# Optimization experiments

Measured on AMD Instinct MI355X. Metric: run time of the kernel, lower is better.

Reference implementation:

```python
import jax, jax.numpy as jnp
import numpy as np

D_MODEL = 256
N_LAYERS = 6
N_HEADS = 8
D_FF = 1024
HEAD_DIM = D_MODEL // N_HEADS
EPS = 1e-5


def layer_norm(x, scale, bias):
    mu = jnp.mean(x, axis=-1, keepdims=True)
    var = jnp.var(x, axis=-1, keepdims=True)
    return (x - mu) * jax.lax.rsqrt(var + EPS) * scale + bias


def setup_inputs() -> dict:
    key = jax.random.key(0)
    ks = jax.random.split(key, 12)
    B, T = 4, 2048
    x = jax.random.normal(ks[0], (B, T, D_MODEL), dtype=jnp.float32)
    L = N_LAYERS
    s = 0.02
    inp = {
        "x": x,
        "ln1_s": jnp.ones((L, D_MODEL), jnp.float32),
        "ln1_b": jnp.zeros((L, D_MODEL), jnp.float32),
        "wq": jax.random.normal(ks[1], (L, D_MODEL, D_MODEL), jnp.float32) * s,
        "bq": jnp.zeros((L, D_MODEL), jnp.float32),
        "wk": jax.random.normal(ks[2], (L, D_MODEL, D_MODEL), jnp.float32) * s,
        "bk": jnp.zeros((L, D_MODEL), jnp.float32),
        "wv": jax.random.normal(ks[3], (L, D_MODEL, D_MODEL), jnp.float32) * s,
        "bv": jnp.zeros((L, D_MODEL), jnp.float32),
        "wo": jax.random.normal(ks[4], (L, D_MODEL, D_MODEL), jnp.float32) * s,
        "bo": jnp.zeros((L, D_MODEL), jnp.float32),
        "ln2_s": jnp.ones((L, D_MODEL), jnp.float32),
        "ln2_b": jnp.zeros((L, D_MODEL), jnp.float32),
        "w1": jax.random.normal(ks[5], (L, D_MODEL, D_FF), jnp.float32) * s,
        "b1": jnp.zeros((L, D_FF), jnp.float32),
        "w2": jax.random.normal(ks[6], (L, D_FF, D_MODEL), jnp.float32) * s,
        "b2": jnp.zeros((L, D_MODEL), jnp.float32),
    }
    return inp


def reference(x, ln1_s, ln1_b, wq, bq, wk, bk, wv, bv, wo, bo, ln2_s, ln2_b, w1, b1, w2, b2):
    B, T, D = x.shape
    scale = 1.0 / jnp.sqrt(jnp.float32(HEAD_DIM))
    for l in range(N_LAYERS):
        normed = layer_norm(x, ln1_s[l], ln1_b[l])
        q = (normed @ wq[l] + bq[l]).reshape(B, T, N_HEADS, HEAD_DIM)
        k = (normed @ wk[l] + bk[l]).reshape(B, T, N_HEADS, HEAD_DIM)
        v = (normed @ wv[l] + bv[l]).reshape(B, T, N_HEADS, HEAD_DIM)
        scores = jnp.einsum('bqhd,bkhd->bhqk', q, k) * scale  # [B,H,T,T]
        attn = jax.nn.softmax(scores, axis=-1)
        attn_out = jnp.einsum('bhqk,bkhd->bqhd', attn, v).reshape(B, T, D)
        x = x + attn_out @ wo[l] + bo[l]
        h = layer_norm(x, ln2_s[l], ln2_b[l])
        h = jax.nn.gelu(h @ w1[l] + b1[l], approximate=False)
        x = x + h @ w2[l] + b2[l]
    return x
```

## Files before the change

kernel.cpp:

```cpp
#include <hip/hip_runtime.h>
#include <math.h>

#define D_MODELC 256
#define N_LAYERSC 6
#define N_HEADSC 8
#define D_FFC 1024
#define HEAD_DIMC 32
#define B_SZ 4
#define T_SEQ 2048
#define M_ROWS 8192
#define QKV_N 768
#define KSPLIT 4

typedef short bf16x8 __attribute__((ext_vector_type(8)));
typedef short bf16x4 __attribute__((ext_vector_type(4)));
typedef float f32x4  __attribute__((ext_vector_type(4)));
typedef unsigned u32x4 __attribute__((ext_vector_type(4)));
typedef unsigned short u16;

#define QSCALE 0.25503488f

#define SWZ(b) ((b) ^ (((b) >> 3) & 0x70))

__device__ __forceinline__ void gload16(const void* g, void* l) {
    __builtin_amdgcn_global_load_lds(
        (const __attribute__((address_space(1))) void*)g,
        (__attribute__((address_space(3))) void*)l, 16, 0, 0);
}

__device__ __forceinline__ u16 f2bf(float x) {
    unsigned u = __builtin_bit_cast(unsigned, x);
    u += 0x7FFF + ((u >> 16) & 1);
    return (u16)(u >> 16);
}

__device__ __forceinline__ float bf2f(short x) {
    return __builtin_bit_cast(float, (unsigned)((u16)x) << 16);
}

__device__ __forceinline__ unsigned pack2bf(float a, float b) {
    return __builtin_amdgcn_perm(__builtin_bit_cast(unsigned, b),
                                 __builtin_bit_cast(unsigned, a), 0x07060302u);
}

__device__ __forceinline__ float fast_gelu(float x) {
    float y  = x * 0.70710678118654752f;
    float ay = __builtin_fabsf(y);
    float t  = __builtin_amdgcn_rcpf(1.0f + 0.3275911f * ay);
    float p  = t * (0.254829592f + t * (-0.284496736f + t * (1.421413741f
               + t * (-1.453152027f + t * 1.061405429f))));
    float e  = __builtin_amdgcn_exp2f(-ay * ay * 1.4426950408889634f);
    float er = 1.0f - p * e;
    er = y < 0.0f ? -er : er;
    return 0.5f * x * (1.0f + er);
}

__device__ __forceinline__ void transpose_tile(
    const float* __restrict__ src, u16* __restrict__ dst,
    int K, int N, int k0, int n0, float scale, float (*ts)[33])
{
    const int r = threadIdx.x >> 3, c4 = (threadIdx.x & 7) * 4;
    const float4 v = *(const float4*)(src + (size_t)(k0 + r) * N + n0 + c4);
    ts[r][c4 + 0] = v.x; ts[r][c4 + 1] = v.y;
    ts[r][c4 + 2] = v.z; ts[r][c4 + 3] = v.w;
    __syncthreads();
    bf16x4 o;
#pragma unroll
    for (int i = 0; i < 4; i++) o[i] = (short)f2bf(ts[c4 + i][r] * scale);
    *(bf16x4*)(dst + (size_t)(n0 + r) * K + k0 + c4) = o;
}

__global__ __launch_bounds__(256) void prep_all(
    const float* __restrict__ wq, const float* __restrict__ wk,
    const float* __restrict__ wv, const float* __restrict__ wo,
    const float* __restrict__ w1, const float* __restrict__ w2,
    const float* __restrict__ bq, const float* __restrict__ bk,
    const float* __restrict__ bv,
    u16* __restrict__ wqkv_t, u16* __restrict__ wo_t,
    u16* __restrict__ w1_t, u16* __restrict__ w2_t,
    float* __restrict__ qkvb,
    const float* __restrict__ x, const float* __restrict__ gamma,
    const float* __restrict__ beta, float* __restrict__ X,
    u16* __restrict__ Y)
{
    __shared__ float ts[32][33];
    const int bid = blockIdx.x;
    if (bid < 1152) {
        const int sec = bid / 384, t = bid % 384;
        const int z = t >> 6, rem = t & 63, ty = rem >> 3, tx = rem & 7;
        const float* src = sec == 0 ? wq : (sec == 1 ? wk : wv);
        transpose_tile(src + (size_t)z * 65536,
                       wqkv_t + (size_t)z * QKV_N * 256 + sec * 256 * 256,
                       256, 256, ty * 32, tx * 32,
                       sec == 0 ? QSCALE : 1.0f, ts);
    } else if (bid < 1536) {
        const int t = bid - 1152;
        const int z = t >> 6, rem = t & 63, ty = rem >> 3, tx = rem & 7;
        transpose_tile(wo + (size_t)z * 65536, wo_t + (size_t)z * 65536,
                       256, 256, ty * 32, tx * 32, 1.0f, ts);
    } else if (bid < 3072) {
        const int t = bid - 1536;
        const int z = t >> 8, rem = t & 255, ty = rem >> 5, tx = rem & 31;
        transpose_tile(w1 + (size_t)z * 262144, w1_t + (size_t)z * 262144,
                       256, D_FFC, ty * 32, tx * 32, 1.0f, ts);
    } else if (bid < 4608) {
        const int t = bid - 3072;
        const int z = t >> 8, rem = t & 255, ty = rem >> 3, tx = rem & 7;
        transpose_tile(w2 + (size_t)z * 262144, w2_t + (size_t)z * 262144,
                       D_FFC, 256, ty * 32, tx * 32, 1.0f, ts);
    } else if (bid < 4626) {
        const int i = (bid - 4608) * 256 + threadIdx.x;
        const int l = i / QKV_N, j = i % QKV_N;
        float v;
        if (j < 256)      v = bq[l * 256 + j] * QSCALE;
        else if (j < 512) v = bk[l * 256 + j - 256];
        else              v = bv[l * 256 + j - 512];
        qkvb[i] = v;
    } else {
        const int w = threadIdx.x >> 6, lane = threadIdx.x & 63;
        const int row = (bid - 4626) * 4 + w;
        const float4 v = *(const float4*)(x + (size_t)row * 256 + lane * 4);
        *(float4*)(X + (size_t)row * 256 + lane * 4) = v;
        float sum = v.x + v.y + v.z + v.w;
        float sq  = v.x * v.x + v.y * v.y + v.z * v.z + v.w * v.w;
#pragma unroll
        for (int off = 32; off > 0; off >>= 1) {
            sum += __shfl_xor(sum, off, 64);
            sq  += __shfl_xor(sq,  off, 64);
        }
        float mu  = sum * (1.0f / 256.0f);
        float var = sq * (1.0f / 256.0f) - mu * mu;
        float rr  = rsqrtf(var + 1e-5f);
        const float4 g  = *(const float4*)(gamma + lane * 4);
        const float4 bb = *(const float4*)(beta + lane * 4);
        bf16x4 o;
        o[0] = (short)f2bf((v.x - mu) * rr * g.x + bb.x);
        o[1] = (short)f2bf((v.y - mu) * rr * g.y + bb.y);
        o[2] = (short)f2bf((v.z - mu) * rr * g.z + bb.z);
        o[3] = (short)f2bf((v.w - mu) * rr * g.w + bb.w);
        *(bf16x4*)(Y + (size_t)row * 256 + lane * 4) = o;
    }
}

template <int EPI>
__global__ __launch_bounds__(256) void mfma_gemm(
    const u16* __restrict__ A, const u16* __restrict__ Bt,
    const float* __restrict__ bias, u16* __restrict__ Vout,
    void* __restrict__ Cout, int N, int K)
{
    __shared__ u16 As[128 * 64];
    __shared__ u16 Bs[128 * 64];
    const int tid = threadIdx.x, w = tid >> 6, lane = tid & 63;
    const int c = lane & 15, quad = lane >> 4;
    const int row0 = blockIdx.y * 128, col0 = blockIdx.x * 128;
    const int wr = w >> 1, wc = w & 1;
    const int cswz = (c & 7) << 4;

    int flv[4], rA[4], colA[4];
#pragma unroll
    for (int ci = 0; ci < 4; ci++) {
        flv[ci]  = (w * 4 + ci) * 1024 + lane * 16;
        const int fsw = SWZ(flv[ci]);
        rA[ci]   = fsw >> 7;
        colA[ci] = (fsw & 127) >> 1;
    }

    f32x4 acc[4][4] = {};

    for (int k0 = 0; k0 < K; k0 += 64) {
        __syncthreads();
#pragma unroll
        for (int ci = 0; ci < 4; ci++) {
            gload16(A  + (size_t)(row0 + rA[ci]) * K + k0 + colA[ci],
                    (char*)As + flv[ci]);
            gload16(Bt + (size_t)(col0 + rA[ci]) * K + k0 + colA[ci],
                    (char*)Bs + flv[ci]);
        }
        __syncthreads();
#pragma unroll
        for (int kk = 0; kk < 2; kk++) {
            bf16x8 af[4], bfv[4];
#pragma unroll
            for (int i = 0; i < 4; i++)
                af[i] = *(const bf16x8*)((const char*)As +
                    ((((wr * 64 + i * 16 + c) * 64 + kk * 32 + quad * 8) * 2) ^ cswz));
#pragma unroll
            for (int j = 0; j < 4; j++)
                bfv[j] = *(const bf16x8*)((const char*)Bs +
                    ((((wc * 64 + j * 16 + c) * 64 + kk * 32 + quad * 8) * 2) ^ cswz));
#pragma unroll
            for (int i = 0; i < 4; i++)
#pragma unroll
                for (int j = 0; j < 4; j++)
                    acc[i][j] = __builtin_amdgcn_mfma_f32_16x16x32_bf16(
                        af[i], bfv[j], acc[i][j], 0, 0, 0);
        }
    }

    float bj[4];
#pragma unroll
    for (int j = 0; j < 4; j++) bj[j] = bias[col0 + wc * 64 + j * 16 + c];

    if (EPI == 3 && col0 >= 512) {
#pragma unroll
        for (int i = 0; i < 4; i++) {
            const int tok = row0 + wr * 64 + i * 16 + quad * 4;
#pragma unroll
            for (int j = 0; j < 4; j++) {
                const int dim = col0 - 512 + wc * 64 + j * 16 + c;
                bf16x4 o;
#pragma unroll
                for (int r = 0; r < 4; r++) o[r] = (short)f2bf(acc[i][j][r] + bj[j]);
                *(bf16x4*)&Vout[(size_t)dim * M_ROWS + tok] = o;
            }
        }
        return;
    }

#pragma unroll
    for (int i = 0; i < 4; i++) {
#pragma unroll
        for (int r = 0; r < 4; r++) {
            const int gr = row0 + wr * 64 + i * 16 + quad * 4 + r;
#pragma unroll
            for (int j = 0; j < 4; j++) {
                const int gc = col0 + wc * 64 + j * 16 + c;
                float v = acc[i][j][r] + bj[j];
                if (EPI == 2) v = fast_gelu(v);
                ((u16*)Cout)[(size_t)gr * N + gc] = f2bf(v);
            }
        }
    }
}

template <int DOLN, int MERGE>
__global__ __launch_bounds__(256) void gemm_ln(
    const u16* __restrict__ A, const float* __restrict__ Lmrg,
    const u16* __restrict__ Bt, const float* __restrict__ bias,
    const float* __restrict__ resid, float* __restrict__ Xout,
    const float* __restrict__ gamma, const float* __restrict__ beta,
    u16* __restrict__ Nout, int K)
{
    __shared__ u16 As[32 * 64];
    __shared__ u16 Bs[256 * 64];
    __shared__ float2 red[4][32];
    const int tid = threadIdx.x, w = tid >> 6, lane = tid & 63;
    const int c = lane & 15, quad = lane >> 4;
    const int row0 = blockIdx.x * 32;
    const int cswz = (c & 7) << 4;

    const int flA  = w * 1024 + lane * 16;
    const int fsA  = SWZ(flA);
    const int rA_m = flA >> 7, colA_m = (flA & 127) >> 1;
    const int rA_g = fsA >> 7, colA_g = (fsA & 127) >> 1;

    int flB[8], rB[8], colB[8];
#pragma unroll
    for (int ci = 0; ci < 8; ci++) {
        flB[ci]  = (w * 8 + ci) * 1024 + lane * 16;
        const int fsB = SWZ(flB[ci]);
        rB[ci]   = fsB >> 7;
        colB[ci] = (fsB & 127) >> 1;
    }

    f32x4 acc[2][4] = {};

    auto loadA = [&](int gc) -> bf16x8 {
        const int row = row0 + rA_m;
        const int head = gc >> 5;
        float ls = 0.f;
#pragma unroll
        for (int p = 0; p < KSPLIT; p++)
            ls += Lmrg[(size_t)p * M_ROWS * 8 + (size_t)row * 8 + head];
        const float inv = __builtin_amdgcn_rcpf(ls);
        float s[8] = {0.f, 0.f, 0.f, 0.f, 0.f, 0.f, 0.f, 0.f};
#pragma unroll
        for (int p = 0; p < KSPLIT; p++) {
            bf16x8 a = *(const bf16x8*)(A + (size_t)p * M_ROWS * 256
                                          + (size_t)row * 256 + gc);
#pragma unroll
            for (int j = 0; j < 8; j++) s[j] += bf2f(a[j]);
        }
        bf16x8 o;
#pragma unroll
        for (int j = 0; j < 8; j++) o[j] = (short)f2bf(s[j] * inv);
        return o;
    };

    bf16x8 pA;
    if (MERGE) pA = loadA(colA_m);

    for (int k0 = 0; k0 < K; k0 += 64) {
        __syncthreads();
#pragma unroll
        for (int ci = 0; ci < 8; ci++)
            gload16(Bt + (size_t)rB[ci] * K + k0 + colB[ci], (char*)Bs + flB[ci]);
        if (MERGE) {
            *(bf16x8*)((char*)As + fsA) = pA;
        } else {
            gload16(A + (size_t)(row0 + rA_g) * K + k0 + colA_g, (char*)As + flA);
        }
        __syncthreads();
        if (MERGE && k0 + 64 < K)
            pA = loadA(k0 + 64 + colA_m);
#pragma unroll
        for (int kk = 0; kk < 2; kk++) {
            bf16x8 af[2], bfv[4];
#pragma unroll
            for (int i = 0; i < 2; i++)
                af[i] = *(const bf16x8*)((const char*)As +
                    ((((i * 16 + c) * 64 + kk * 32 + quad * 8) * 2) ^ cswz));
#pragma unroll
            for (int j = 0; j < 4; j++)
                bfv[j] = *(const bf16x8*)((const char*)Bs +
                    ((((w * 64 + j * 16 + c) * 64 + kk * 32 + quad * 8) * 2) ^ cswz));
#pragma unroll
            for (int i = 0; i < 2; i++)
#pragma unroll
                for (int j = 0; j < 4; j++)
                    acc[i][j] = __builtin_amdgcn_mfma_f32_16x16x32_bf16(
                        af[i], bfv[j], acc[i][j], 0, 0, 0);
        }
    }

    float bj[4];
#pragma unroll
    for (int j = 0; j < 4; j++) bj[j] = bias[w * 64 + j * 16 + c];
    float xv[2][4][4];
#pragma unroll
    for (int i = 0; i < 2; i++)
#pragma unroll
        for (int r = 0; r < 4; r++) {
            const int gr = row0 + i * 16 + quad * 4 + r;
#pragma unroll
            for (int j = 0; j < 4; j++) {
                const int gc = w * 64 + j * 16 + c;
                xv[i][j][r] = acc[i][j][r] + bj[j] + resid[(size_t)gr * 256 + gc];
            }
        }

    if (DOLN) {
        float sm[2][4], sp[2][4];
#pragma unroll
        for (int i = 0; i < 2; i++)
#pragma unroll
            for (int r = 0; r < 4; r++) {
                float s = 0.f, q = 0.f;
#pragma unroll
                for (int j = 0; j < 4; j++) { s += xv[i][j][r]; q += xv[i][j][r] * xv[i][j][r]; }
                sm[i][r] = s; sp[i][r] = q;
            }
#pragma unroll
        for (int off = 1; off < 16; off <<= 1)
#pragma unroll
            for (int i = 0; i < 2; i++)
#pragma unroll
                for (int r = 0; r < 4; r++) {
                    sm[i][r] += __shfl_xor(sm[i][r], off, 64);
                    sp[i][r] += __shfl_xor(sp[i][r], off, 64);
                }
        __syncthreads();
        if (c == 0) {
#pragma unroll
            for (int i = 0; i < 2; i++)
#pragma unroll
                for (int r = 0; r < 4; r++)
                    red[w][i * 16 + quad * 4 + r] = make_float2(sm[i][r], sp[i][r]);
        }
        __syncthreads();
#pragma unroll
        for (int i = 0; i < 2; i++)
#pragma unroll
            for (int r = 0; r < 4; r++) {
                const int row = i * 16 + quad * 4 + r;
                float2 t0 = red[0][row], t1 = red[1][row];
                float2 t2 = red[2][row], t3 = red[3][row];
                float S = (t0.x + t1.x) + (t2.x + t3.x);
                float Q = (t0.y + t1.y) + (t2.y + t3.y);
                float mu = S * (1.0f / 256.0f);
                float var = Q * (1.0f / 256.0f) - mu * mu;
                float rr = rsqrtf(var + 1e-5f);
                const int gr = row0 + row;
#pragma unroll
                for (int j = 0; j < 4; j++) {
                    const int gc = w * 64 + j * 16 + c;
                    float x = xv[i][j][r];
                    Xout[(size_t)gr * 256 + gc] = x;
                    Nout[(size_t)gr * 256 + gc] =
                        f2bf((x - mu) * rr * gamma[gc] + beta[gc]);
                }
            }
    } else {
#pragma unroll
        for (int i = 0; i < 2; i++)
#pragma unroll
            for (int r = 0; r < 4; r++) {
                const int gr = row0 + i * 16 + quad * 4 + r;
#pragma unroll
                for (int j = 0; j < 4; j++)
                    Xout[(size_t)gr * 256 + w * 64 + j * 16 + c] = xv[i][j][r];
            }
    }
}

__global__ __launch_bounds__(256) void attn_kernel(
    const u16* __restrict__ QKV, const u16* __restrict__ VT,
    u16* __restrict__ PO, float* __restrict__ Lp)
{
    const int h = blockIdx.y, b = blockIdx.z;
    const int part = blockIdx.x & (KSPLIT - 1);
    const int q0 = (blockIdx.x >> 2) * 128;
    const int tid = threadIdx.x, w = tid >> 6, lane = tid & 63;
    const int c = lane & 15, quad = lane >> 4;

    __shared__ u16 Kf[4096];
    __shared__ u16 Vf[4096];

    const u16* qp = QKV + (size_t)(b * T_SEQ + q0 + w * 32 + c) * QKV_N + h * 32 + quad * 8;
    bf16x8 aQ0 = *(const bf16x8*)qp;
    bf16x8 aQ1 = *(const bf16x8*)(qp + 16 * QKV_N);

    const bf16x8 bOnes = {0x3F80, 0x3F80, 0x3F80, 0x3F80,
                          0x3F80, 0x3F80, 0x3F80, 0x3F80};

    f32x4 O[2][2] = {};
    f32x4 Ol0 = {0.f, 0.f, 0.f, 0.f}, Ol1 = {0.f, 0.f, 0.f, 0.f};

    const u16* kgp = QKV + (size_t)(b * T_SEQ + w * 16 + c) * QKV_N + 256 + h * 32 + quad * 8;
    const u16* vgp = VT + ((size_t)h * 32 + (lane & 31)) * M_ROWS + b * T_SEQ
                     + (w * 2 + (lane >> 5)) * 8;
    u16* kfw = Kf + w * 512 + lane * 8;

    const int vd  = lane & 31, vdh = vd >> 4, vc = vd & 15, vhi = lane >> 5;
    const int vkh = w >> 1, vseg = w & 1;
    const int voff = ((((vkh * 2 + vdh) * 4 + 2 * vhi) * 16 + vc) * 8) + vseg * 4;

    const int kbeg = part * (T_SEQ / KSPLIT);
    const int kend = kbeg + T_SEQ / KSPLIT;

    bf16x8 gK0 = *(const bf16x8*)(kgp + (size_t)kbeg * QKV_N);
    bf16x8 gK1 = *(const bf16x8*)(kgp + (size_t)(kbeg + 64) * QKV_N);
    bf16x8 gV0 = *(const bf16x8*)(vgp + kbeg);
    bf16x8 gV1 = *(const bf16x8*)(vgp + kbeg + 64);

    for (int k0 = kbeg; k0 < kend; k0 += 128) {
        __syncthreads();
        *(bf16x8*)kfw          = gK0;
        *(bf16x8*)(kfw + 2048) = gK1;
        {
            bf16x4 l0v = __builtin_shufflevector(gV0, gV0, 0, 1, 2, 3);
            bf16x4 h0v = __builtin_shufflevector(gV0, gV0, 4, 5, 6, 7);
            bf16x4 l1v = __builtin_shufflevector(gV1, gV1, 0, 1, 2, 3);
            bf16x4 h1v = __builtin_shufflevector(gV1, gV1, 4, 5, 6, 7);
            *(bf16x4*)&Vf[voff]              = l0v;
            *(bf16x4*)&Vf[voff + 128]        = h0v;
            *(bf16x4*)&Vf[2048 + voff]       = l1v;
            *(bf16x4*)&Vf[2048 + voff + 128] = h1v;
        }
        __syncthreads();
        if (k0 + 128 < kend) {
            gK0 = *(const bf16x8*)(kgp + (size_t)(k0 + 128) * QKV_N);
            gK1 = *(const bf16x8*)(kgp + (size_t)(k0 + 192) * QKV_N);
            gV0 = *(const bf16x8*)(vgp + k0 + 128);
            gV1 = *(const bf16x8*)(vgp + k0 + 192);
        }

#pragma unroll
        for (int hf = 0; hf < 2; hf++) {
            const u16* Kb = Kf + hf * 2048;
            const u16* Vb = Vf + hf * 2048;

            unsigned pk0[4][2], pk1[4][2];
#pragma unroll
            for (int g = 0; g < 4; g++) {
                bf16x8 aK = *(const bf16x8*)&Kb[g * 512 + lane * 8];
                f32x4 S0 = __builtin_amdgcn_mfma_f32_16x16x32_bf16(
                    aK, aQ0, (f32x4){0.f, 0.f, 0.f, 0.f}, 0, 0, 0);
                f32x4 S1 = __builtin_amdgcn_mfma_f32_16x16x32_bf16(
                    aK, aQ1, (f32x4){0.f, 0.f, 0.f, 0.f}, 0, 0, 0);
                pk0[g][0] = pack2bf(__builtin_amdgcn_exp2f(S0[0]),
                                    __builtin_amdgcn_exp2f(S0[1]));
                pk0[g][1] = pack2bf(__builtin_amdgcn_exp2f(S0[2]),
                                    __builtin_amdgcn_exp2f(S0[3]));
                pk1[g][0] = pack2bf(__builtin_amdgcn_exp2f(S1[0]),
                                    __builtin_amdgcn_exp2f(S1[1]));
                pk1[g][1] = pack2bf(__builtin_amdgcn_exp2f(S1[2]),
                                    __builtin_amdgcn_exp2f(S1[3]));
            }

            __builtin_amdgcn_s_setprio(1);
#pragma unroll
            for (int kh = 0; kh < 2; kh++) {
                bf16x8 aP0 = __builtin_bit_cast(bf16x8,
                    (u32x4){pk0[2 * kh][0], pk0[2 * kh][1],
                            pk0[2 * kh + 1][0], pk0[2 * kh + 1][1]});
                bf16x8 aP1 = __builtin_bit_cast(bf16x8,
                    (u32x4){pk1[2 * kh][0], pk1[2 * kh][1],
                            pk1[2 * kh + 1][0], pk1[2 * kh + 1][1]});
                Ol0 = __builtin_amdgcn_mfma_f32_16x16x32_bf16(aP0, bOnes, Ol0, 0, 0, 0);
                Ol1 = __builtin_amdgcn_mfma_f32_16x16x32_bf16(aP1, bOnes, Ol1, 0, 0, 0);
#pragma unroll
                for (int dh = 0; dh < 2; dh++) {
                    bf16x8 bV = *(const bf16x8*)&Vb[((kh * 2 + dh) * 64 + lane) * 8];
                    O[0][dh] = __builtin_amdgcn_mfma_f32_16x16x32_bf16(aP0, bV, O[0][dh], 0, 0, 0);
                    O[1][dh] = __builtin_amdgcn_mfma_f32_16x16x32_bf16(aP1, bV, O[1][dh], 0, 0, 0);
                }
            }
            __builtin_amdgcn_s_setprio(0);
        }
    }

    u16* pb = PO + (size_t)part * M_ROWS * 256
              + (size_t)(b * T_SEQ + q0 + w * 32) * 256 + h * 32;
    if (c == 0) {
        float* lb = Lp + (size_t)part * M_ROWS * 8
                    + (size_t)(b * T_SEQ + q0 + w * 32) * 8 + h;
#pragma unroll
        for (int r = 0; r < 4; r++) {
            lb[(size_t)(quad * 4 + r) * 8]      = Ol0[r];
            lb[(size_t)(16 + quad * 4 + r) * 8] = Ol1[r];
        }
    }
#pragma unroll
    for (int r = 0; r < 4; r++) {
        int src = quad * 4 + r;
        pb[(size_t)src * 256 + c]             = f2bf(O[0][0][r]);
        pb[(size_t)src * 256 + 16 + c]        = f2bf(O[0][1][r]);
        pb[(size_t)(16 + src) * 256 + c]      = f2bf(O[1][0][r]);
        pb[(size_t)(16 + src) * 256 + 16 + c] = f2bf(O[1][1][r]);
    }
}

extern "C" void kernel_launch(void* const* d_in, const int* in_sizes, int n_in,
                              void* d_out, int out_size, void* d_ws, size_t ws_size,
                              hipStream_t stream)
{
    const float* x     = (const float*)d_in[0];
    const float* ln1_s = (const float*)d_in[1];
    const float* ln1_b = (const float*)d_in[2];
    const float* wq    = (const float*)d_in[3];
    const float* bq    = (const float*)d_in[4];
    const float* wk    = (const float*)d_in[5];
    const float* bk    = (const float*)d_in[6];
    const float* wv    = (const float*)d_in[7];
    const float* bv    = (const float*)d_in[8];
    const float* wo    = (const float*)d_in[9];
    const float* bo    = (const float*)d_in[10];
    const float* ln2_s = (const float*)d_in[11];
    const float* ln2_b = (const float*)d_in[12];
    const float* w1    = (const float*)d_in[13];
    const float* b1    = (const float*)d_in[14];
    const float* w2    = (const float*)d_in[15];
    const float* b2    = (const float*)d_in[16];

    float* X = (float*)d_out;

    u16* normed = (u16*)d_ws;
    u16* qkv    = normed + (size_t)M_ROWS * 256;
    u16* PO4    = qkv + (size_t)M_ROWS * QKV_N;
    u16* h1     = qkv;
    u16* wqkv_t = PO4 + (size_t)KSPLIT * M_ROWS * 256;
    u16* wo_t   = wqkv_t + (size_t)N_LAYERSC * QKV_N * 256;
    u16* w1_t   = wo_t + (size_t)N_LAYERSC * 256 * 256;
    u16* w2_t   = w1_t + (size_t)N_LAYERSC * D_FFC * 256;
    float* qkvb = (float*)(w2_t + (size_t)N_LAYERSC * 256 * D_FFC);
    u16* VTb    = (u16*)(qkvb + N_LAYERSC * QKV_N);
    float* Lp   = (float*)(VTb + (size_t)256 * M_ROWS);

    dim3 blk(256);

    prep_all<<<dim3(4626 + M_ROWS / 4), blk, 0, stream>>>(
        wq, wk, wv, wo, w1, w2, bq, bk, bv,
        wqkv_t, wo_t, w1_t, w2_t, qkvb,
        x, ln1_s, ln1_b, X, normed);

    dim3 g_qkv(QKV_N / 128, M_ROWS / 128);
    dim3 g_ff(D_FFC / 128, M_ROWS / 128);
    dim3 g_ln32(M_ROWS / 32);
    dim3 g_attn(KSPLIT * T_SEQ / 128, N_HEADSC, B_SZ);

    for (int l = 0; l < N_LAYERSC; l++) {
        mfma_gemm<3><<<g_qkv, blk, 0, stream>>>(
            normed, wqkv_t + (size_t)l * QKV_N * 256, qkvb + l * QKV_N,
            VTb, qkv, QKV_N, 256);
        attn_kernel<<<g_attn, blk, 0, stream>>>(qkv, VTb, PO4, Lp);
        gemm_ln<1, 1><<<g_ln32, blk, 0, stream>>>(
            PO4, Lp, wo_t + (size_t)l * 256 * 256, bo + l * 256, X,
            X, ln2_s + l * 256, ln2_b + l * 256, VTb, 256);
        mfma_gemm<2><<<g_ff, blk, 0, stream>>>(
            VTb, w1_t + (size_t)l * D_FFC * 256, b1 + l * D_FFC,
            nullptr, h1, D_FFC, 256);
        if (l + 1 < N_LAYERSC) {
            gemm_ln<1, 0><<<g_ln32, blk, 0, stream>>>(
                h1, nullptr, w2_t + (size_t)l * 256 * D_FFC,
                b2 + l * 256, X, X, ln1_s + (l + 1) * 256,
                ln1_b + (l + 1) * 256, normed, D_FFC);
        } else {
            gemm_ln<0, 0><<<g_ln32, blk, 0, stream>>>(
                h1, nullptr, w2_t + (size_t)l * 256 * D_FFC,
                b2 + l * 256, X, X, nullptr, nullptr, nullptr, D_FFC);
        }
    }
}
```

Before: 625.8 us.

## Halve attention KV split and widen gemm_ln blocks to 512 threads

Reduces the attention key split from 4 to 2 partitions, halving the partial-output buffer that the output-projection GEMM must read and merge. Separately, gemm_ln now runs with 8 waves per 32-row block, each wave covering 32 output columns instead of 64. This aims to cut merge traffic and raise latency hiding in the LN-fused GEMMs. The cost is fewer attention blocks, with each doing twice the KV work, and an 8-way LN reduction in shared memory.

```diff
diff --git a/kernel.cpp b/kernel.cpp
--- a/kernel.cpp
+++ b/kernel.cpp
@@ -10,7 +10,7 @@
 #define T_SEQ 2048
 #define M_ROWS 8192
 #define QKV_N 768
-#define KSPLIT 4
+#define KSPLIT 2
 
 typedef short bf16x8 __attribute__((ext_vector_type(8)));
 typedef short bf16x4 __attribute__((ext_vector_type(4)));
@@ -234,7 +234,7 @@
 }
 
 template <int DOLN, int MERGE>
-__global__ __launch_bounds__(256) void gemm_ln(
+__global__ __launch_bounds__(512) void gemm_ln(
     const u16* __restrict__ A, const float* __restrict__ Lmrg,
     const u16* __restrict__ Bt, const float* __restrict__ bias,
     const float* __restrict__ resid, float* __restrict__ Xout,
@@ -243,27 +243,28 @@
 {
     __shared__ u16 As[32 * 64];
     __shared__ u16 Bs[256 * 64];
-    __shared__ float2 red[4][32];
+    __shared__ float2 red[8][32];
     const int tid = threadIdx.x, w = tid >> 6, lane = tid & 63;
     const int c = lane & 15, quad = lane >> 4;
     const int row0 = blockIdx.x * 32;
     const int cswz = (c & 7) << 4;
 
-    const int flA  = w * 1024 + lane * 16;
+    const int flA  = tid * 16;
+    const bool doA = tid < 256;
     const int fsA  = SWZ(flA);
     const int rA_m = flA >> 7, colA_m = (flA & 127) >> 1;
     const int rA_g = fsA >> 7, colA_g = (fsA & 127) >> 1;
 
-    int flB[8], rB[8], colB[8];
-#pragma unroll
-    for (int ci = 0; ci < 8; ci++) {
-        flB[ci]  = (w * 8 + ci) * 1024 + lane * 16;
+    int flB[4], rB[4], colB[4];
+#pragma unroll
+    for (int ci = 0; ci < 4; ci++) {
+        flB[ci]  = (w * 4 + ci) * 1024 + lane * 16;
         const int fsB = SWZ(flB[ci]);
         rB[ci]   = fsB >> 7;
         colB[ci] = (fsB & 127) >> 1;
     }
 
-    f32x4 acc[2][4] = {};
+    f32x4 acc[2][2] = {};
 
     auto loadA = [&](int gc) -> bf16x8 {
         const int row = row0 + rA_m;
@@ -288,53 +289,54 @@
     };
 
     bf16x8 pA;
-    if (MERGE) pA = loadA(colA_m);
+    if (MERGE && doA) pA = loadA(colA_m);
 
     for (int k0 = 0; k0 < K; k0 += 64) {
         __syncthreads();
 #pragma unroll
-        for (int ci = 0; ci < 8; ci++)
+        for (int ci = 0; ci < 4; ci++)
             gload16(Bt + (size_t)rB[ci] * K + k0 + colB[ci], (char*)Bs + flB[ci]);
         if (MERGE) {
-            *(bf16x8*)((char*)As + fsA) = pA;
+            if (doA) *(bf16x8*)((char*)As + fsA) = pA;
         } else {
-            gload16(A + (size_t)(row0 + rA_g) * K + k0 + colA_g, (char*)As + flA);
-        }
-        __syncthreads();
-        if (MERGE && k0 + 64 < K)
+            if (doA) gload16(A + (size_t)(row0 + rA_g) * K + k0 + colA_g,
+                             (char*)As + flA);
+        }
+        __syncthreads();
+        if (MERGE && doA && k0 + 64 < K)
             pA = loadA(k0 + 64 + colA_m);
 #pragma unroll
         for (int kk = 0; kk < 2; kk++) {
-            bf16x8 af[2], bfv[4];
+            bf16x8 af[2], bfv[2];
 #pragma unroll
             for (int i = 0; i < 2; i++)
                 af[i] = *(const bf16x8*)((const char*)As +
                     ((((i * 16 + c) * 64 + kk * 32 + quad * 8) * 2) ^ cswz));
 #pragma unroll
-            for (int j = 0; j < 4; j++)
+            for (int j = 0; j < 2; j++)
                 bfv[j] = *(const bf16x8*)((const char*)Bs +
-                    ((((w * 64 + j * 16 + c) * 64 + kk * 32 + quad * 8) * 2) ^ cswz));
+                    ((((w * 32 + j * 16 + c) * 64 + kk * 32 + quad * 8) * 2) ^ cswz));
 #pragma unroll
             for (int i = 0; i < 2; i++)
 #pragma unroll
-                for (int j = 0; j < 4; j++)
+                for (int j = 0; j < 2; j++)
                     acc[i][j] = __builtin_amdgcn_mfma_f32_16x16x32_bf16(
                         af[i], bfv[j], acc[i][j], 0, 0, 0);
         }
     }
 
-    float bj[4];
-#pragma unroll
-    for (int j = 0; j < 4; j++) bj[j] = bias[w * 64 + j * 16 + c];
-    float xv[2][4][4];
+    float bj[2];
+#pragma unroll
+    for (int j = 0; j < 2; j++) bj[j] = bias[w * 32 + j * 16 + c];
+    float xv[2][2][4];
 #pragma unroll
     for (int i = 0; i < 2; i++)
 #pragma unroll
         for (int r = 0; r < 4; r++) {
             const int gr = row0 + i * 16 + quad * 4 + r;
 #pragma unroll
-            for (int j = 0; j < 4; j++) {
-                const int gc = w * 64 + j * 16 + c;
+            for (int j = 0; j < 2; j++) {
+                const int gc = w * 32 + j * 16 + c;
                 xv[i][j][r] = acc[i][j][r] + bj[j] + resid[(size_t)gr * 256 + gc];
             }
         }
@@ -347,7 +349,7 @@
             for (int r = 0; r < 4; r++) {
                 float s = 0.f, q = 0.f;
 #pragma unroll
-                for (int j = 0; j < 4; j++) { s += xv[i][j][r]; q += xv[i][j][r] * xv[i][j][r]; }
+                for (int j = 0; j < 2; j++) { s += xv[i][j][r]; q += xv[i][j][r] * xv[i][j][r]; }
                 sm[i][r] = s; sp[i][r] = q;
             }
 #pragma unroll
@@ -373,17 +375,19 @@
 #pragma unroll
             for (int r = 0; r < 4; r++) {
                 const int row = i * 16 + quad * 4 + r;
-                float2 t0 = red[0][row], t1 = red[1][row];
-                float2 t2 = red[2][row], t3 = red[3][row];
-                float S = (t0.x + t1.x) + (t2.x + t3.x);
-                float Q = (t0.y + t1.y) + (t2.y + t3.y);
+                float S = 0.f, Q = 0.f;
+#pragma unroll
+                for (int wp = 0; wp < 8; wp++) {
+                    S += red[wp][row].x;
+                    Q += red[wp][row].y;
+                }
                 float mu = S * (1.0f / 256.0f);
                 float var = Q * (1.0f / 256.0f) - mu * mu;
                 float rr = rsqrtf(var + 1e-5f);
                 const int gr = row0 + row;
 #pragma unroll
-                for (int j = 0; j < 4; j++) {
-                    const int gc = w * 64 + j * 16 + c;
+                for (int j = 0; j < 2; j++) {
+                    const int gc = w * 32 + j * 16 + c;
                     float x = xv[i][j][r];
                     Xout[(size_t)gr * 256 + gc] = x;
                     Nout[(size_t)gr * 256 + gc] =
@@ -397,8 +401,8 @@
             for (int r = 0; r < 4; r++) {
                 const int gr = row0 + i * 16 + quad * 4 + r;
 #pragma unroll
-                for (int j = 0; j < 4; j++)
-                    Xout[(size_t)gr * 256 + w * 64 + j * 16 + c] = xv[i][j][r];
+                for (int j = 0; j < 2; j++)
+                    Xout[(size_t)gr * 256 + w * 32 + j * 16 + c] = xv[i][j][r];
             }
     }
 }
@@ -409,7 +413,7 @@
 {
     const int h = blockIdx.y, b = blockIdx.z;
     const int part = blockIdx.x & (KSPLIT - 1);
-    const int q0 = (blockIdx.x >> 2) * 128;
+    const int q0 = (blockIdx.x >> 1) * 128;
     const int tid = threadIdx.x, w = tid >> 6, lane = tid & 63;
     const int c = lane & 15, quad = lane >> 4;
 
@@ -557,9 +561,9 @@
 
     u16* normed = (u16*)d_ws;
     u16* qkv    = normed + (size_t)M_ROWS * 256;
-    u16* PO4    = qkv + (size_t)M_ROWS * QKV_N;
+    u16* PO2    = qkv + (size_t)M_ROWS * QKV_N;
     u16* h1     = qkv;
-    u16* wqkv_t = PO4 + (size_t)KSPLIT * M_ROWS * 256;
+    u16* wqkv_t = PO2 + (size_t)KSPLIT * M_ROWS * 256;
     u16* wo_t   = wqkv_t + (size_t)N_LAYERSC * QKV_N * 256;
     u16* w1_t   = wo_t + (size_t)N_LAYERSC * 256 * 256;
     u16* w2_t   = w1_t + (size_t)N_LAYERSC * D_FFC * 256;
@@ -567,7 +571,7 @@
     u16* VTb    = (u16*)(qkvb + N_LAYERSC * QKV_N);
     float* Lp   = (float*)(VTb + (size_t)256 * M_ROWS);
 
-    dim3 blk(256);
+    dim3 blk(256), blk512(512);
 
     prep_all<<<dim3(4626 + M_ROWS / 4), blk, 0, stream>>>(
         wq, wk, wv, wo, w1, w2, bq, bk, bv,
@@ -583,20 +587,20 @@
         mfma_gemm<3><<<g_qkv, blk, 0, stream>>>(
             normed, wqkv_t + (size_t)l * QKV_N * 256, qkvb + l * QKV_N,
             VTb, qkv, QKV_N, 256);
-        attn_kernel<<<g_attn, blk, 0, stream>>>(qkv, VTb, PO4, Lp);
-        gemm_ln<1, 1><<<g_ln32, blk, 0, stream>>>(
-            PO4, Lp, wo_t + (size_t)l * 256 * 256, bo + l * 256, X,
+        attn_kernel<<<g_attn, blk, 0, stream>>>(qkv, VTb, PO2, Lp);
+        gemm_ln<1, 1><<<g_ln32, blk512, 0, stream>>>(
+            PO2, Lp, wo_t + (size_t)l * 256 * 256, bo + l * 256, X,
             X, ln2_s + l * 256, ln2_b + l * 256, VTb, 256);
         mfma_gemm<2><<<g_ff, blk, 0, stream>>>(
             VTb, w1_t + (size_t)l * D_FFC * 256, b1 + l * D_FFC,
             nullptr, h1, D_FFC, 256);
         if (l + 1 < N_LAYERSC) {
-            gemm_ln<1, 0><<<g_ln32, blk, 0, stream>>>(
+            gemm_ln<1, 0><<<g_ln32, blk512, 0, stream>>>(
                 h1, nullptr, w2_t + (size_t)l * 256 * D_FFC,
                 b2 + l * 256, X, X, ln1_s + (l + 1) * 256,
                 ln1_b + (l + 1) * 256, normed, D_FFC);
         } else {
-            gemm_ln<0, 0><<<g_ln32, blk, 0, stream>>>(
+            gemm_ln<0, 0><<<g_ln32, blk512, 0, stream>>>(
                 h1, nullptr, w2_t + (size_t)l * 256 * D_FFC,
                 b2 + l * 256, X, X, nullptr, nullptr, nullptr, D_FFC);
         }
```

Measured after the change: 614.8 us. Within noise of the previous version (-1.8%).

## Halve attention KV split and shrink gemm_ln row tile to 16

Applied to the files above, without the earlier changes.

Attention now splits the key range in two parts instead of four, which halves the partial output and log-sum buffers that the merged output-projection GEMM has to read and combine. The fused GEMM+LayerNorm kernel now handles 16 rows per block instead of 32, doubling the grid to 512 blocks so more CUs are busy. The cost is that each block reuses the 256-wide weight tile over fewer rows, and only half the threads load A. Attention also exposes less parallelism per head.

```diff
diff --git a/kernel.cpp b/kernel.cpp
--- a/kernel.cpp
+++ b/kernel.cpp
@@ -10,7 +10,7 @@
 #define T_SEQ 2048
 #define M_ROWS 8192
 #define QKV_N 768
-#define KSPLIT 4
+#define KSPLIT 2
 
 typedef short bf16x8 __attribute__((ext_vector_type(8)));
 typedef short bf16x4 __attribute__((ext_vector_type(4)));
@@ -241,15 +241,16 @@
     const float* __restrict__ gamma, const float* __restrict__ beta,
     u16* __restrict__ Nout, int K)
 {
-    __shared__ u16 As[32 * 64];
+    __shared__ u16 As[16 * 64];
     __shared__ u16 Bs[256 * 64];
-    __shared__ float2 red[4][32];
+    __shared__ float2 red[4][16];
     const int tid = threadIdx.x, w = tid >> 6, lane = tid & 63;
     const int c = lane & 15, quad = lane >> 4;
-    const int row0 = blockIdx.x * 32;
+    const int row0 = blockIdx.x * 16;
     const int cswz = (c & 7) << 4;
 
-    const int flA  = w * 1024 + lane * 16;
+    const int flA  = tid * 16;
+    const bool doA = tid < 128;
     const int fsA  = SWZ(flA);
     const int rA_m = flA >> 7, colA_m = (flA & 127) >> 1;
     const int rA_g = fsA >> 7, colA_g = (fsA & 127) >> 1;
@@ -263,7 +264,7 @@
         colB[ci] = (fsB & 127) >> 1;
     }
 
-    f32x4 acc[2][4] = {};
+    f32x4 acc[4] = {};
 
     auto loadA = [&](int gc) -> bf16x8 {
         const int row = row0 + rA_m;
@@ -288,7 +289,7 @@
     };
 
     bf16x8 pA;
-    if (MERGE) pA = loadA(colA_m);
+    if (MERGE && doA) pA = loadA(colA_m);
 
     for (int k0 = 0; k0 < K; k0 += 64) {
         __syncthreads();
@@ -296,110 +297,95 @@
         for (int ci = 0; ci < 8; ci++)
             gload16(Bt + (size_t)rB[ci] * K + k0 + colB[ci], (char*)Bs + flB[ci]);
         if (MERGE) {
-            *(bf16x8*)((char*)As + fsA) = pA;
+            if (doA) *(bf16x8*)((char*)As + fsA) = pA;
         } else {
-            gload16(A + (size_t)(row0 + rA_g) * K + k0 + colA_g, (char*)As + flA);
-        }
-        __syncthreads();
-        if (MERGE && k0 + 64 < K)
+            if (doA) gload16(A + (size_t)(row0 + rA_g) * K + k0 + colA_g,
+                             (char*)As + flA);
+        }
+        __syncthreads();
+        if (MERGE && doA && k0 + 64 < K)
             pA = loadA(k0 + 64 + colA_m);
 #pragma unroll
         for (int kk = 0; kk < 2; kk++) {
-            bf16x8 af[2], bfv[4];
-#pragma unroll
-            for (int i = 0; i < 2; i++)
-                af[i] = *(const bf16x8*)((const char*)As +
-                    ((((i * 16 + c) * 64 + kk * 32 + quad * 8) * 2) ^ cswz));
+            bf16x8 af, bfv[4];
+            af = *(const bf16x8*)((const char*)As +
+                (((c * 64 + kk * 32 + quad * 8) * 2) ^ cswz));
 #pragma unroll
             for (int j = 0; j < 4; j++)
                 bfv[j] = *(const bf16x8*)((const char*)Bs +
                     ((((w * 64 + j * 16 + c) * 64 + kk * 32 + quad * 8) * 2) ^ cswz));
 #pragma unroll
-            for (int i = 0; i < 2; i++)
-#pragma unroll
-                for (int j = 0; j < 4; j++)
-                    acc[i][j] = __builtin_amdgcn_mfma_f32_16x16x32_bf16(
-                        af[i], bfv[j], acc[i][j], 0, 0, 0);
+            for (int j = 0; j < 4; j++)
+                acc[j] = __builtin_amdgcn_mfma_f32_16x16x32_bf16(
+                    af, bfv[j], acc[j], 0, 0, 0);
         }
     }
 
     float bj[4];
 #pragma unroll
     for (int j = 0; j < 4; j++) bj[j] = bias[w * 64 + j * 16 + c];
-    float xv[2][4][4];
-#pragma unroll
-    for (int i = 0; i < 2; i++)
+    float xv[4][4];
+#pragma unroll
+    for (int r = 0; r < 4; r++) {
+        const int gr = row0 + quad * 4 + r;
+#pragma unroll
+        for (int j = 0; j < 4; j++) {
+            const int gc = w * 64 + j * 16 + c;
+            xv[j][r] = acc[j][r] + bj[j] + resid[(size_t)gr * 256 + gc];
+        }
+    }
+
+    if (DOLN) {
+        float sm[4], sp[4];
 #pragma unroll
         for (int r = 0; r < 4; r++) {
-            const int gr = row0 + i * 16 + quad * 4 + r;
+            float s = 0.f, q = 0.f;
+#pragma unroll
+            for (int j = 0; j < 4; j++) { s += xv[j][r]; q += xv[j][r] * xv[j][r]; }
+            sm[r] = s; sp[r] = q;
+        }
+#pragma unroll
+        for (int off = 1; off < 16; off <<= 1)
+#pragma unroll
+            for (int r = 0; r < 4; r++) {
+                sm[r] += __shfl_xor(sm[r], off, 64);
+                sp[r] += __shfl_xor(sp[r], off, 64);
+            }
+        __syncthreads();
+        if (c == 0) {
+#pragma unroll
+            for (int r = 0; r < 4; r++)
+                red[w][quad * 4 + r] = make_float2(sm[r], sp[r]);
+        }
+        __syncthreads();
+#pragma unroll
+        for (int r = 0; r < 4; r++) {
+            const int row = quad * 4 + r;
+            float2 t0 = red[0][row], t1 = red[1][row];
+            float2 t2 = red[2][row], t3 = red[3][row];
+            float S = (t0.x + t1.x) + (t2.x + t3.x);
+            float Q = (t0.y + t1.y) + (t2.y + t3.y);
+            float mu = S * (1.0f / 256.0f);
+            float var = Q * (1.0f / 256.0f) - mu * mu;
+            float rr = rsqrtf(var + 1e-5f);
+            const int gr = row0 + row;
 #pragma unroll
             for (int j = 0; j < 4; j++) {
                 const int gc = w * 64 + j * 16 + c;
-                xv[i][j][r] = acc[i][j][r] + bj[j] + resid[(size_t)gr * 256 + gc];
+                float x = xv[j][r];
+                Xout[(size_t)gr * 256 + gc] = x;
+                Nout[(size_t)gr * 256 + gc] =
+                    f2bf((x - mu) * rr * gamma[gc] + beta[gc]);
             }
         }
-
-    if (DOLN) {
-        float sm[2][4], sp[2][4];
-#pragma unroll
-        for (int i = 0; i < 2; i++)
-#pragma unroll
-            for (int r = 0; r < 4; r++) {
-                float s = 0.f, q = 0.f;
-#pragma unroll
-                for (int j = 0; j < 4; j++) { s += xv[i][j][r]; q += xv[i][j][r] * xv[i][j][r]; }
-                sm[i][r] = s; sp[i][r] = q;
-            }
-#pragma unroll
-        for (int off = 1; off < 16; off <<= 1)
-#pragma unroll
-            for (int i = 0; i < 2; i++)
-#pragma unroll
-                for (int r = 0; r < 4; r++) {
-                    sm[i][r] += __shfl_xor(sm[i][r], off, 64);
-                    sp[i][r] += __shfl_xor(sp[i][r], off, 64);
-                }
-        __syncthreads();
-        if (c == 0) {
-#pragma unroll
-            for (int i = 0; i < 2; i++)
-#pragma unroll
-                for (int r = 0; r < 4; r++)
-                    red[w][i * 16 + quad * 4 + r] = make_float2(sm[i][r], sp[i][r]);
-        }
-        __syncthreads();
-#pragma unroll
-        for (int i = 0; i < 2; i++)
-#pragma unroll
-            for (int r = 0; r < 4; r++) {
-                const int row = i * 16 + quad * 4 + r;
-                float2 t0 = red[0][row], t1 = red[1][row];
-                float2 t2 = red[2][row], t3 = red[3][row];
-                float S = (t0.x + t1.x) + (t2.x + t3.x);
-                float Q = (t0.y + t1.y) + (t2.y + t3.y);
-                float mu = S * (1.0f / 256.0f);
-                float var = Q * (1.0f / 256.0f) - mu * mu;
-                float rr = rsqrtf(var + 1e-5f);
-                const int gr = row0 + row;
-#pragma unroll
-                for (int j = 0; j < 4; j++) {
-                    const int gc = w * 64 + j * 16 + c;
-                    float x = xv[i][j][r];
-                    Xout[(size_t)gr * 256 + gc] = x;
-                    Nout[(size_t)gr * 256 + gc] =
-                        f2bf((x - mu) * rr * gamma[gc] + beta[gc]);
-                }
-            }
     } else {
 #pragma unroll
-        for (int i = 0; i < 2; i++)
-#pragma unroll
-            for (int r = 0; r < 4; r++) {
-                const int gr = row0 + i * 16 + quad * 4 + r;
-#pragma unroll
-                for (int j = 0; j < 4; j++)
-                    Xout[(size_t)gr * 256 + w * 64 + j * 16 + c] = xv[i][j][r];
-            }
+        for (int r = 0; r < 4; r++) {
+            const int gr = row0 + quad * 4 + r;
+#pragma unroll
+            for (int j = 0; j < 4; j++)
+                Xout[(size_t)gr * 256 + w * 64 + j * 16 + c] = xv[j][r];
+        }
     }
 }
 
@@ -409,7 +395,7 @@
 {
     const int h = blockIdx.y, b = blockIdx.z;
     const int part = blockIdx.x & (KSPLIT - 1);
-    const int q0 = (blockIdx.x >> 2) * 128;
+    const int q0 = (blockIdx.x >> 1) * 128;
     const int tid = threadIdx.x, w = tid >> 6, lane = tid & 63;
     const int c = lane & 15, quad = lane >> 4;
 
@@ -557,9 +543,9 @@
 
     u16* normed = (u16*)d_ws;
     u16* qkv    = normed + (size_t)M_ROWS * 256;
-    u16* PO4    = qkv + (size_t)M_ROWS * QKV_N;
+    u16* PO2    = qkv + (size_t)M_ROWS * QKV_N;
     u16* h1     = qkv;
-    u16* wqkv_t = PO4 + (size_t)KSPLIT * M_ROWS * 256;
+    u16* wqkv_t = PO2 + (size_t)KSPLIT * M_ROWS * 256;
     u16* wo_t   = wqkv_t + (size_t)N_LAYERSC * QKV_N * 256;
     u16* w1_t   = wo_t + (size_t)N_LAYERSC * 256 * 256;
     u16* w2_t   = w1_t + (size_t)N_LAYERSC * D_FFC * 256;
@@ -576,27 +562,27 @@
 
     dim3 g_qkv(QKV_N / 128, M_ROWS / 128);
     dim3 g_ff(D_FFC / 128, M_ROWS / 128);
-    dim3 g_ln32(M_ROWS / 32);
+    dim3 g_ln16(M_ROWS / 16);
     dim3 g_attn(KSPLIT * T_SEQ / 128, N_HEADSC, B_SZ);
 
     for (int l = 0; l < N_LAYERSC; l++) {
         mfma_gemm<3><<<g_qkv, blk, 0, stream>>>(
             normed, wqkv_t + (size_t)l * QKV_N * 256, qkvb + l * QKV_N,
             VTb, qkv, QKV_N, 256);
-        attn_kernel<<<g_attn, blk, 0, stream>>>(qkv, VTb, PO4, Lp);
-        gemm_ln<1, 1><<<g_ln32, blk, 0, stream>>>(
-            PO4, Lp, wo_t + (size_t)l * 256 * 256, bo + l * 256, X,
+        attn_kernel<<<g_attn, blk, 0, stream>>>(qkv, VTb, PO2, Lp);
+        gemm_ln<1, 1><<<g_ln16, blk, 0, stream>>>(
+            PO2, Lp, wo_t + (size_t)l * 256 * 256, bo + l * 256, X,
             X, ln2_s + l * 256, ln2_b + l * 256, VTb, 256);
         mfma_gemm<2><<<g_ff, blk, 0, stream>>>(
             VTb, w1_t + (size_t)l * D_FFC * 256, b1 + l * D_FFC,
             nullptr, h1, D_FFC, 256);
         if (l + 1 < N_LAYERSC) {
-            gemm_ln<1, 0><<<g_ln32, blk, 0, stream>>>(
+            gemm_ln<1, 0><<<g_ln16, blk, 0, stream>>>(
                 h1, nullptr, w2_t + (size_t)l * 256 * D_FFC,
                 b2 + l * 256, X, X, ln1_s + (l + 1) * 256,
                 ln1_b + (l + 1) * 256, normed, D_FFC);
         } else {
-            gemm_ln<0, 0><<<g_ln32, blk, 0, stream>>>(
+            gemm_ln<0, 0><<<g_ln16, blk, 0, stream>>>(
                 h1, nullptr, w2_t + (size_t)l * 256 * D_FFC,
                 b2 + l * 256, X, X, nullptr, nullptr, nullptr, D_FFC);
         }
```

After: 600.8 us. -4.0%, faster.
